# Performance work log

Hardware: AMD Instinct MI355X
Metric: run time of the kernel (lower is better)

The kernel has to match this reference:

```python
import jax, jax.numpy as jnp
import numpy as np

N_NODES = 100000
N_EDGES = 1280000
N_PAIRS = 500000
IN_CH = 64
HID = 64
OUT_CH = 1


def setup_inputs() -> dict:
    key = jax.random.key(0)
    ks = jax.random.split(key, 16)
    s = lambda fan_in: 1.0 / np.sqrt(fan_in)
    return {
        "x": jax.random.normal(ks[0], (N_NODES, IN_CH), dtype=jnp.float32),
        "edge_index": jax.random.randint(ks[1], (2, N_EDGES), 0, N_NODES, dtype=jnp.int32),
        "edge_pairs": jax.random.randint(ks[2], (N_PAIRS, 2), 0, N_NODES, dtype=jnp.int32),
        "W1l": jax.random.normal(ks[3], (IN_CH, HID), dtype=jnp.float32) * s(IN_CH),
        "b1l": jnp.zeros((HID,), dtype=jnp.float32),
        "W1r": jax.random.normal(ks[4], (IN_CH, HID), dtype=jnp.float32) * s(IN_CH),
        "W2l": jax.random.normal(ks[5], (HID, HID), dtype=jnp.float32) * s(HID),
        "b2l": jnp.zeros((HID,), dtype=jnp.float32),
        "W2r": jax.random.normal(ks[6], (HID, HID), dtype=jnp.float32) * s(HID),
        "Wr1": jax.random.normal(ks[7], (2 * HID, 64), dtype=jnp.float32) * s(2 * HID),
        "br1": jnp.zeros((64,), dtype=jnp.float32),
        "Wr2": jax.random.normal(ks[8], (64, OUT_CH), dtype=jnp.float32) * s(64),
        "br2": jnp.zeros((OUT_CH,), dtype=jnp.float32),
    }


def sage_conv(x, src, dst, Wl, bl, Wr, num_nodes):
    # PyG SAGEConv (aggr='mean'): out = lin_l(mean_{j in N(i)} x_j) + lin_r(x_i)
    msg = x[src]                                            # [E, C] gather
    agg = jax.ops.segment_sum(msg, dst, num_segments=num_nodes)  # [N, C]
    cnt = jax.ops.segment_sum(jnp.ones_like(dst, dtype=x.dtype), dst,
                              num_segments=num_nodes)       # [N]
    mean = agg / jnp.maximum(cnt, 1.0)[:, None]             # nodes w/o neighbors -> 0
    return mean @ Wl + bl + x @ Wr


def reference(x, edge_index, edge_pairs, W1l, b1l, W1r, W2l, b2l, W2r,
              Wr1, br1, Wr2, br2):
    n = x.shape[0]
    src, dst = edge_index[0], edge_index[1]
    h = jax.nn.relu(sage_conv(x, src, dst, W1l, b1l, W1r, n))
    h = jax.nn.relu(sage_conv(h, src, dst, W2l, b2l, W2r, n))
    h_pair = jnp.concatenate([h[edge_pairs[:, 0]], h[edge_pairs[:, 1]]], axis=1)  # [P, 2H]
    return jax.nn.relu(h_pair @ Wr1 + br1) @ Wr2 + br2
```

## Files before the change

kernel.cpp:

```cpp
#include <hip/hip_runtime.h>
#include <stdint.h>

#define N_NODES 100000
#define N_EDGES 1280000
#define N_PAIRS 500000
#define ELL_STRIDE 48
#define NXCD 8

typedef _Float16 half_t;
typedef __attribute__((ext_vector_type(8))) _Float16 half8;
typedef __attribute__((ext_vector_type(4))) float f32x4;

union H8U { half8 h; int u[4]; };

__global__ void init_all_kernel(int* __restrict__ cursor, int* __restrict__ zrow, int N,
                                const float* __restrict__ W1l, const float* __restrict__ W1r,
                                const float* __restrict__ W2l, const float* __restrict__ W2r,
                                const float* __restrict__ Wr1, half_t* __restrict__ Bt) {
  int t = blockIdx.x * blockDim.x + threadIdx.x;
  if (t < N) cursor[t] = 0;
  if (t < 32) zrow[t] = 0;
  if (t < 3 * 128 * 64) {
    int g = t >> 13, rem = t & 8191;
    int n = rem >> 6, k = rem & 63;
    const float* B;
    if (g == 0) B = (n < 64) ? W1l : W1r;
    else if (g == 1) B = (n < 64) ? W2l : W2r;
    else B = (n < 64) ? Wr1 : (Wr1 + 64 * 64);
    Bt[t] = (half_t)B[k * 64 + (n & 63)];
  }
}

__global__ void fill_xcd_kernel(const int* __restrict__ src, const int* __restrict__ dst,
                                int* __restrict__ cursor, int* __restrict__ adj, int E) {
  const int xcd = blockIdx.x & (NXCD - 1);
  const int chunk = blockIdx.x >> 3;
  const int step = (N_NODES + NXCD - 1) / NXCD;
  const int lo = xcd * step;
  const int hi = min(N_NODES, lo + step);
  const int base = chunk * 2048 + threadIdx.x * 4;

  #pragma unroll
  for (int half = 0; half < 2; ++half) {
    int e0 = base + half * 1024;
    if (e0 + 3 < E) {
      int4 d4 = *(const int4*)&dst[e0];
      int dv[4] = {d4.x, d4.y, d4.z, d4.w};
      #pragma unroll
      for (int i = 0; i < 4; ++i) {
        int d = dv[i];
        if (d >= lo && d < hi) {
          int pos = atomicAdd(&cursor[d], 1);
          if (pos < ELL_STRIDE) adj[(size_t)d * ELL_STRIDE + pos] = src[e0 + i] << 7;
        }
      }
    } else {
      for (int i = 0; i < 4; ++i) {
        int e = e0 + i;
        if (e < E) {
          int d = dst[e];
          if (d >= lo && d < hi) {
            int pos = atomicAdd(&cursor[d], 1);
            if (pos < ELL_STRIDE) adj[(size_t)d * ELL_STRIDE + pos] = src[e] << 7;
          }
        }
      }
    }
  }
}

template <bool AHALF>
__global__ __launch_bounds__(256) void gemm_mfma(
    const void* __restrict__ Av, const half_t* __restrict__ Bt,
    half_t* __restrict__ C1, half_t* __restrict__ C2, int M) {
  const int tid = threadIdx.x;
  const int wave = tid >> 6, l = tid & 63;
  const int lr = l & 15;
  const int kg = l >> 4;
  const int m_base = blockIdx.x * 128 + wave * 32;

  half8 a[2][2];
  #pragma unroll
  for (int mt = 0; mt < 2; ++mt) {
    int row = m_base + mt * 16 + lr;
    row = min(row, M - 1);
    if (AHALF) {
      const half_t* A = (const half_t*)Av;
      #pragma unroll
      for (int ks = 0; ks < 2; ++ks)
        a[mt][ks] = *(const half8*)&A[(size_t)row * 64 + ks * 32 + kg * 8];
    } else {
      const float* A = (const float*)Av;
      #pragma unroll
      for (int ks = 0; ks < 2; ++ks) {
        float4 f0 = *(const float4*)&A[(size_t)row * 64 + ks * 32 + kg * 8];
        float4 f1 = *(const float4*)&A[(size_t)row * 64 + ks * 32 + kg * 8 + 4];
        half8 h;
        h[0] = (half_t)f0.x; h[1] = (half_t)f0.y; h[2] = (half_t)f0.z; h[3] = (half_t)f0.w;
        h[4] = (half_t)f1.x; h[5] = (half_t)f1.y; h[6] = (half_t)f1.z; h[7] = (half_t)f1.w;
        a[mt][ks] = h;
      }
    }
  }

  f32x4 acc[2][8];
  #pragma unroll
  for (int mt = 0; mt < 2; ++mt)
    #pragma unroll
    for (int nt = 0; nt < 8; ++nt) acc[mt][nt] = (f32x4)(0.f);

  #pragma unroll
  for (int nt = 0; nt < 8; ++nt) {
    half8 b0 = *(const half8*)&Bt[(size_t)(nt * 16 + lr) * 64 + kg * 8];
    half8 b1 = *(const half8*)&Bt[(size_t)(nt * 16 + lr) * 64 + 32 + kg * 8];
    #pragma unroll
    for (int mt = 0; mt < 2; ++mt) {
      acc[mt][nt] = __builtin_amdgcn_mfma_f32_16x16x32_f16(a[mt][0], b0, acc[mt][nt], 0, 0, 0);
      acc[mt][nt] = __builtin_amdgcn_mfma_f32_16x16x32_f16(a[mt][1], b1, acc[mt][nt], 0, 0, 0);
    }
  }

  #pragma unroll
  for (int mt = 0; mt < 2; ++mt) {
    #pragma unroll
    for (int r = 0; r < 4; ++r) {
      int row = m_base + mt * 16 + kg * 4 + r;
      if (row < M) {
        #pragma unroll
        for (int nt = 0; nt < 4; ++nt)
          C1[(size_t)row * 64 + nt * 16 + lr] = (half_t)acc[mt][nt][r];
        #pragma unroll
        for (int nt = 4; nt < 8; ++nt)
          C2[(size_t)row * 64 + (nt - 4) * 16 + lr] = (half_t)acc[mt][nt][r];
      }
    }
  }
}

__global__ __launch_bounds__(256) void agg_kernel(
    const half_t* __restrict__ Qh, const half_t* __restrict__ Pt,
    const int* __restrict__ cnt, const int* __restrict__ adj,
    const float* __restrict__ bias, half_t* __restrict__ Hh, int N) {
  int lane = threadIdx.x & 63;
  int node = blockIdx.x * 8 + ((threadIdx.x >> 6) << 1) + (lane >> 5);
  if (node >= N) return;
  int sub = lane & 31;
  int g = sub >> 3;
  int cb = (sub & 7) * 8;
  const int4* arow4 = (const int4*)(adj + (size_t)node * ELL_STRIDE);
  const int ZOFF = N * 128;
  const char* Qb = (const char*)Qh + cb * 2;

  int4 q0 = arow4[g];
  int4 q1 = arow4[4 + g];
  int deg = cnt[node];
  half8 ph = *(const half8*)&Pt[(size_t)node * 64 + cb];

  int m = min(deg, ELL_STRIDE);
  int s0 = g * 4;
  int o0 = (s0 + 0 < m) ? q0.x : ZOFF;
  int o1 = (s0 + 1 < m) ? q0.y : ZOFF;
  int o2 = (s0 + 2 < m) ? q0.z : ZOFF;
  int o3 = (s0 + 3 < m) ? q0.w : ZOFF;

  half8 w0 = *(const half8*)(Qb + o0);
  half8 w1 = *(const half8*)(Qb + o1);
  half8 w2 = *(const half8*)(Qb + o2);
  half8 w3 = *(const half8*)(Qb + o3);
  w0 += w1; w2 += w3;

  H8U a;
  a.h = w0 + w2;

  if (deg > 16) {
    int s1 = 16 + g * 4;
    int o4 = (s1 + 0 < m) ? q1.x : ZOFF;
    int o5 = (s1 + 1 < m) ? q1.y : ZOFF;
    int o6 = (s1 + 2 < m) ? q1.z : ZOFF;
    int o7 = (s1 + 3 < m) ? q1.w : ZOFF;
    half8 w4 = *(const half8*)(Qb + o4);
    half8 w5 = *(const half8*)(Qb + o5);
    half8 w6 = *(const half8*)(Qb + o6);
    half8 w7 = *(const half8*)(Qb + o7);
    w4 += w5; w6 += w7;
    a.h += w4 + w6;

    if (deg > 32) {
      int4 q2 = arow4[8 + g];
      int s2 = 32 + g * 4;
      int t0 = (s2 + 0 < m) ? q2.x : ZOFF;
      int t1 = (s2 + 1 < m) ? q2.y : ZOFF;
      int t2 = (s2 + 2 < m) ? q2.z : ZOFF;
      int t3 = (s2 + 3 < m) ? q2.w : ZOFF;
      half8 u0 = *(const half8*)(Qb + t0);
      half8 u1 = *(const half8*)(Qb + t1);
      half8 u2 = *(const half8*)(Qb + t2);
      half8 u3 = *(const half8*)(Qb + t3);
      u0 += u1; u2 += u3;
      a.h += u0 + u2;
    }
  }

  {
    H8U b;
    #pragma unroll
    for (int k = 0; k < 4; ++k) b.u[k] = __shfl_down(a.u[k], 8);
    a.h += b.h;
    #pragma unroll
    for (int k = 0; k < 4; ++k) b.u[k] = __shfl_down(a.u[k], 16);
    a.h += b.h;
  }

  if (sub < 8) {
    float inv = 1.f / fmaxf((float)deg, 1.f);
    float4 ba = *(const float4*)&bias[cb];
    float4 bb = *(const float4*)&bias[cb + 4];
    float bs[8] = {ba.x, ba.y, ba.z, ba.w, bb.x, bb.y, bb.z, bb.w};
    half8 o;
    #pragma unroll
    for (int i = 0; i < 8; ++i) {
      float v = (float)a.h[i] * inv + (float)ph[i] + bs[i];
      o[i] = (half_t)fmaxf(v, 0.f);
    }
    *(half8*)&Hh[(size_t)node * 64 + cb] = o;
  }
}

__global__ __launch_bounds__(256) void pair_kernel(
    const half_t* __restrict__ Uh, const half_t* __restrict__ Vh, const int* __restrict__ pairs,
    const float* __restrict__ br1, const float* __restrict__ Wr2, const float* __restrict__ br2,
    float* __restrict__ out, int P) {
  int wave = blockIdx.x * 4 + (threadIdx.x >> 6);
  int lane = threadIdx.x & 63;
  int h = lane >> 4;
  int sub = lane & 15;
  int side = sub >> 3;
  int cb = (sub & 7) * 8;
  int pA = wave * 8 + h;
  int pB = pA + 4;
  if (pA >= P) return;

  int2 prA = *(const int2*)&pairs[2 * pA];
  int2 prB = (pB < P) ? *(const int2*)&pairs[2 * pB] : prA;
  int nodeA = side ? prA.y : prA.x;
  int nodeB = side ? prB.y : prB.x;
  const half_t* T = side ? Vh : Uh;
  H8U a, c;
  a.h = *(const half8*)&T[(size_t)nodeA * 64 + cb];
  c.h = *(const half8*)&T[(size_t)nodeB * 64 + cb];

  H8U b;
  #pragma unroll
  for (int k = 0; k < 4; ++k) b.u[k] = __shfl_down(a.u[k], 8);
  a.h += b.h;
  #pragma unroll
  for (int k = 0; k < 4; ++k) b.u[k] = __shfl_down(c.u[k], 8);
  c.h += b.h;

  float4 b0 = *(const float4*)&br1[cb];
  float4 b1 = *(const float4*)&br1[cb + 4];
  float4 w0 = *(const float4*)&Wr2[cb];
  float4 w1 = *(const float4*)&Wr2[cb + 4];

  float rA = 0.f, rB = 0.f;
  if (side == 0) {
    rA = fmaxf((float)a.h[0] + b0.x, 0.f) * w0.x + fmaxf((float)a.h[1] + b0.y, 0.f) * w0.y
       + fmaxf((float)a.h[2] + b0.z, 0.f) * w0.z + fmaxf((float)a.h[3] + b0.w, 0.f) * w0.w
       + fmaxf((float)a.h[4] + b1.x, 0.f) * w1.x + fmaxf((float)a.h[5] + b1.y, 0.f) * w1.y
       + fmaxf((float)a.h[6] + b1.z, 0.f) * w1.z + fmaxf((float)a.h[7] + b1.w, 0.f) * w1.w;
    rB = fmaxf((float)c.h[0] + b0.x, 0.f) * w0.x + fmaxf((float)c.h[1] + b0.y, 0.f) * w0.y
       + fmaxf((float)c.h[2] + b0.z, 0.f) * w0.z + fmaxf((float)c.h[3] + b0.w, 0.f) * w0.w
       + fmaxf((float)c.h[4] + b1.x, 0.f) * w1.x + fmaxf((float)c.h[5] + b1.y, 0.f) * w1.y
       + fmaxf((float)c.h[6] + b1.z, 0.f) * w1.z + fmaxf((float)c.h[7] + b1.w, 0.f) * w1.w;
  }
  rA += __shfl_xor(rA, 1);
  rA += __shfl_xor(rA, 2);
  rA += __shfl_xor(rA, 4);
  rB += __shfl_xor(rB, 1);
  rB += __shfl_xor(rB, 2);
  rB += __shfl_xor(rB, 4);
  if (sub == 0) {
    out[pA] = rA + br2[0];
    if (pB < P) out[pB] = rB + br2[0];
  }
}

extern "C" void kernel_launch(void* const* d_in, const int* in_sizes, int n_in,
                              void* d_out, int out_size, void* d_ws, size_t ws_size,
                              hipStream_t stream) {
  const float* x   = (const float*)d_in[0];
  const int*   ei  = (const int*)d_in[1];
  const int* pairs = (const int*)d_in[2];
  const float* W1l = (const float*)d_in[3];
  const float* b1l = (const float*)d_in[4];
  const float* W1r = (const float*)d_in[5];
  const float* W2l = (const float*)d_in[6];
  const float* b2l = (const float*)d_in[7];
  const float* W2r = (const float*)d_in[8];
  const float* Wr1 = (const float*)d_in[9];
  const float* br1 = (const float*)d_in[10];
  const float* Wr2 = (const float*)d_in[11];
  const float* br2 = (const float*)d_in[12];
  float* out = (float*)d_out;

  const int N = N_NODES, E = N_EDGES, P = N_PAIRS;
  const int* srcI = ei;
  const int* dstI = ei + E;

  char* w = (char*)d_ws;
  int* cursor = (int*)w;  w += (size_t)N * 4;
  w = (char*)(((uintptr_t)w + 255) & ~(uintptr_t)255);
  int* adj = (int*)w;     w += (size_t)N * ELL_STRIDE * 4;
  w = (char*)(((uintptr_t)w + 255) & ~(uintptr_t)255);
  half_t* Qh = (half_t*)w; w += (size_t)(N + 1) * 64 * 2;
  w = (char*)(((uintptr_t)w + 255) & ~(uintptr_t)255);
  half_t* Pt = (half_t*)w; w += (size_t)N * 64 * 2;
  w = (char*)(((uintptr_t)w + 255) & ~(uintptr_t)255);
  half_t* Hh = (half_t*)w; w += (size_t)N * 64 * 2;
  w = (char*)(((uintptr_t)w + 255) & ~(uintptr_t)255);
  half_t* Bt = (half_t*)w; w += (size_t)3 * 128 * 64 * 2;
  half_t* Vh = Pt;

  init_all_kernel<<<(N + 255) / 256, 256, 0, stream>>>(
      cursor, (int*)(Qh + (size_t)N * 64), N, W1l, W1r, W2l, W2r, Wr1, Bt);

  {
    const int chunks = (E + 2047) / 2048;
    fill_xcd_kernel<<<chunks * NXCD, 256, 0, stream>>>(srcI, dstI, cursor, adj, E);
  }

  const int GB = (N + 127) / 128;
  gemm_mfma<false><<<GB, 256, 0, stream>>>((const void*)x, Bt, Qh, Pt, N);
  agg_kernel<<<(N + 7) / 8, 256, 0, stream>>>(Qh, Pt, cursor, adj, b1l, Hh, N);
  gemm_mfma<true><<<GB, 256, 0, stream>>>((const void*)Hh, Bt + 8192, Qh, Pt, N);
  agg_kernel<<<(N + 7) / 8, 256, 0, stream>>>(Qh, Pt, cursor, adj, b2l, Hh, N);
  gemm_mfma<true><<<GB, 256, 0, stream>>>((const void*)Hh, Bt + 16384, Qh, Vh, N);
  pair_kernel<<<(P + 31) / 32, 256, 0, stream>>>(Qh, Vh, pairs, br1, Wr2, br2, out, P);
}
```

Baseline: 194.7 us.

## Transpose ELL adjacency to slot-major layout for coalesced neighbor loads

```diff
diff --git a/kernel.cpp b/kernel.cpp
--- a/kernel.cpp
+++ b/kernel.cpp
@@ -51,7 +51,7 @@
         int d = dv[i];
         if (d >= lo && d < hi) {
           int pos = atomicAdd(&cursor[d], 1);
-          if (pos < ELL_STRIDE) adj[(size_t)d * ELL_STRIDE + pos] = src[e0 + i] << 7;
+          if (pos < ELL_STRIDE) adj[(size_t)pos * N_NODES + d] = src[e0 + i] << 7;
         }
       }
     } else {
@@ -61,7 +61,7 @@
           int d = dst[e];
           if (d >= lo && d < hi) {
             int pos = atomicAdd(&cursor[d], 1);
-            if (pos < ELL_STRIDE) adj[(size_t)d * ELL_STRIDE + pos] = src[e] << 7;
+            if (pos < ELL_STRIDE) adj[(size_t)pos * N_NODES + d] = src[e] << 7;
           }
         }
       }
@@ -147,21 +147,23 @@
   int sub = lane & 31;
   int g = sub >> 3;
   int cb = (sub & 7) * 8;
-  const int4* arow4 = (const int4*)(adj + (size_t)node * ELL_STRIDE);
+  const int* ap = adj + node;
   const int ZOFF = N * 128;
   const char* Qb = (const char*)Qh + cb * 2;
 
-  int4 q0 = arow4[g];
-  int4 q1 = arow4[4 + g];
+  int s0 = g * 4;
+  int q0x = ap[(size_t)(s0 + 0) * N];
+  int q0y = ap[(size_t)(s0 + 1) * N];
+  int q0z = ap[(size_t)(s0 + 2) * N];
+  int q0w = ap[(size_t)(s0 + 3) * N];
   int deg = cnt[node];
   half8 ph = *(const half8*)&Pt[(size_t)node * 64 + cb];
 
   int m = min(deg, ELL_STRIDE);
-  int s0 = g * 4;
-  int o0 = (s0 + 0 < m) ? q0.x : ZOFF;
-  int o1 = (s0 + 1 < m) ? q0.y : ZOFF;
-  int o2 = (s0 + 2 < m) ? q0.z : ZOFF;
-  int o3 = (s0 + 3 < m) ? q0.w : ZOFF;
+  int o0 = (s0 + 0 < m) ? q0x : ZOFF;
+  int o1 = (s0 + 1 < m) ? q0y : ZOFF;
+  int o2 = (s0 + 2 < m) ? q0z : ZOFF;
+  int o3 = (s0 + 3 < m) ? q0w : ZOFF;
 
   half8 w0 = *(const half8*)(Qb + o0);
   half8 w1 = *(const half8*)(Qb + o1);
@@ -174,10 +176,14 @@
 
   if (deg > 16) {
     int s1 = 16 + g * 4;
-    int o4 = (s1 + 0 < m) ? q1.x : ZOFF;
-    int o5 = (s1 + 1 < m) ? q1.y : ZOFF;
-    int o6 = (s1 + 2 < m) ? q1.z : ZOFF;
-    int o7 = (s1 + 3 < m) ? q1.w : ZOFF;
+    int q1x = ap[(size_t)(s1 + 0) * N];
+    int q1y = ap[(size_t)(s1 + 1) * N];
+    int q1z = ap[(size_t)(s1 + 2) * N];
+    int q1w = ap[(size_t)(s1 + 3) * N];
+    int o4 = (s1 + 0 < m) ? q1x : ZOFF;
+    int o5 = (s1 + 1 < m) ? q1y : ZOFF;
+    int o6 = (s1 + 2 < m) ? q1z : ZOFF;
+    int o7 = (s1 + 3 < m) ? q1w : ZOFF;
     half8 w4 = *(const half8*)(Qb + o4);
     half8 w5 = *(const half8*)(Qb + o5);
     half8 w6 = *(const half8*)(Qb + o6);
@@ -186,12 +192,15 @@
     a.h += w4 + w6;
 
     if (deg > 32) {
-      int4 q2 = arow4[8 + g];
       int s2 = 32 + g * 4;
-      int t0 = (s2 + 0 < m) ? q2.x : ZOFF;
-      int t1 = (s2 + 1 < m) ? q2.y : ZOFF;
-      int t2 = (s2 + 2 < m) ? q2.z : ZOFF;
-      int t3 = (s2 + 3 < m) ? q2.w : ZOFF;
+      int q2x = ap[(size_t)(s2 + 0) * N];
+      int q2y = ap[(size_t)(s2 + 1) * N];
+      int q2z = ap[(size_t)(s2 + 2) * N];
+      int q2w = ap[(size_t)(s2 + 3) * N];
+      int t0 = (s2 + 0 < m) ? q2x : ZOFF;
+      int t1 = (s2 + 1 < m) ? q2y : ZOFF;
+      int t2 = (s2 + 2 < m) ? q2z : ZOFF;
+      int t3 = (s2 + 3 < m) ? q2w : ZOFF;
       half8 u0 = *(const half8*)(Qb + t0);
       half8 u1 = *(const half8*)(Qb + t1);
       half8 u2 = *(const half8*)(Qb + t2);
```

Measured after the change: 202.4 us. +4.0%, slower.
